# Optimization experiments

Hardware: AMD Instinct MI355X
Metric: run time of the kernel (lower is better)

Reference implementation:

```python
import jax, jax.numpy as jnp
import numpy as np

N, E, M = 100000, 3200000, 1000000  # nodes, message edges, scored move edges
DIN, H = 128, 64


def setup_inputs() -> dict:
    key = jax.random.key(0)
    ks = jax.random.split(key, 20)
    rn = lambda k, shape, s=0.05: (jax.random.normal(k, shape, jnp.float32) * s)
    return {
        "x": jax.random.normal(ks[0], (N, DIN), jnp.float32),
        "edge_index": jax.random.randint(ks[1], (2, E), 0, N, jnp.int64),
        "move_edge_index": jax.random.randint(ks[2], (2, M), 0, N, jnp.int64),
        "lin1_w": rn(ks[3], (DIN, H)), "lin1_b": jnp.zeros((H,), jnp.float32),
        "lin2_w": rn(ks[4], (H, H)), "lin2_b": jnp.zeros((H,), jnp.float32),
        "conv1_wl": rn(ks[5], (H, H)), "conv1_bl": jnp.zeros((H,), jnp.float32),
        "conv1_wr": rn(ks[6], (H, H)),
        "conv2_wl": rn(ks[7], (H, H)), "conv2_bl": jnp.zeros((H,), jnp.float32),
        "conv2_wr": rn(ks[8], (H, H)),
        "mlp_w1": rn(ks[9], (2 * H, H)), "mlp_b1": jnp.zeros((H,), jnp.float32),
        "mlp_w2": rn(ks[10], (H, 1)), "mlp_b2": jnp.zeros((1,), jnp.float32),
    }


def reference(x, edge_index, move_edge_index,
              lin1_w, lin1_b, lin2_w, lin2_b,
              conv1_wl, conv1_bl, conv1_wr,
              conv2_wl, conv2_bl, conv2_wr,
              mlp_w1, mlp_b1, mlp_w2, mlp_b2):
    n = x.shape[0]
    src, dst = edge_index[0], edge_index[1]
    # mean-aggregation degrees (PyG SAGEConv default aggr='mean'; isolated nodes -> 0)
    deg = jax.ops.segment_sum(jnp.ones(src.shape, x.dtype), dst, num_segments=n)
    inv_deg = (jnp.where(deg > 0, 1.0 / jnp.maximum(deg, 1.0), 0.0))[:, None]

    def sage(h, wl, bl, wr):
        # out = W_l @ mean_j h_j + b_l + W_r @ h_i
        agg = jax.ops.segment_sum(h[src], dst, num_segments=n) * inv_deg
        return agg @ wl + bl + h @ wr

    h = jax.nn.relu(x @ lin1_w + lin1_b)
    h = jax.nn.relu(sage(h, conv1_wl, conv1_bl, conv1_wr))
    h = jax.nn.relu(h @ lin2_w + lin2_b)
    h = jax.nn.relu(sage(h, conv2_wl, conv2_bl, conv2_wr))

    # edge scoring: gather src/dst embeddings, concat, 2-layer MLP, tanh
    cat = jnp.concatenate([h[move_edge_index[0]], h[move_edge_index[1]]], axis=1)  # [M, 2H]
    logits = (jax.nn.relu(cat @ mlp_w1 + mlp_b1) @ mlp_w2 + mlp_b2).reshape(-1)
    return jnp.tanh(logits)
```

## Files before the change

kernel.cpp:

```cpp
#include <hip/hip_runtime.h>
#include <math.h>

#define MAXB 512
#define PART_BS 1024
#define NBLK_MAX 248
#define CAPB 96

typedef _Float16 f16;
typedef __attribute__((ext_vector_type(2))) _Float16 f16x2;
typedef __attribute__((ext_vector_type(4))) _Float16 f16x4;
typedef __attribute__((ext_vector_type(8))) _Float16 f16x8;
typedef __attribute__((ext_vector_type(4))) float f32x4;

static __device__ __forceinline__ unsigned short f2h(float f) {
    f16 h = (f16)f; return *(unsigned short*)&h;
}

__global__ __launch_bounds__(PART_BS) void k_part(
    const int* __restrict__ src, const int* __restrict__ dst,
    unsigned* __restrict__ bb, int* __restrict__ cnt,
    const float* __restrict__ lin1_w, const float* __restrict__ c1_wl,
    const float* __restrict__ c1_wr, const float* __restrict__ lin2_w,
    const float* __restrict__ c2_wl, const float* __restrict__ c2_wr,
    const float* __restrict__ mlp_w1, const float* __restrict__ mlp_w2,
    unsigned short* __restrict__ Wt,
    int E, int shift, int pcap, int nblk, int nb) {
    __shared__ int h[MAXB];
    const int blk = blockIdx.x;
    for (int i = blk * PART_BS + (int)threadIdx.x; i < 36928; i += gridDim.x * PART_BS) {
        float v;
        if (i < 8192)       { int j = i;         int n = j >> 7, k = j & 127; v = lin1_w[k * 64 + n]; }
        else if (i < 16384) { int j = i - 8192;  int n = j >> 7, k = j & 127;
                              v = (k < 64) ? c1_wl[k * 64 + n] : c1_wr[(k - 64) * 64 + n]; }
        else if (i < 20480) { int j = i - 16384; int n = j >> 6, k = j & 63;  v = lin2_w[k * 64 + n]; }
        else if (i < 28672) { int j = i - 20480; int n = j >> 7, k = j & 127;
                              v = (k < 64) ? c2_wl[k * 64 + n] : c2_wr[(k - 64) * 64 + n]; }
        else if (i < 32768) { int j = i - 28672; int n = j >> 6, k = j & 63;  v = mlp_w1[k * 64 + n]; }
        else if (i < 36864) { int j = i - 32768; int n = j >> 6, k = j & 63;  v = mlp_w1[(k + 64) * 64 + n]; }
        else                { v = mlp_w2[i - 36864]; }
        Wt[i] = f2h(v);
    }
    const int b0 = blk * pcap;
    const int e1 = min(b0 + pcap, E);
    for (int i = threadIdx.x; i < MAXB; i += PART_BS) h[i] = 0;
    __syncthreads();
    const unsigned mask = (1u << shift) - 1u;
    for (int pos = b0 + (int)threadIdx.x * 8; pos < e1; pos += PART_BS * 8) {
        if (pos + 8 <= e1) {
            int4 d0 = *(const int4*)(dst + pos), d1 = *(const int4*)(dst + pos + 4);
            int4 s0 = *(const int4*)(src + pos), s1 = *(const int4*)(src + pos + 4);
            int dd[8] = {d0.x, d0.y, d0.z, d0.w, d1.x, d1.y, d1.z, d1.w};
            int ss[8] = {s0.x, s0.y, s0.z, s0.w, s1.x, s1.y, s1.z, s1.w};
#pragma unroll
            for (int k = 0; k < 8; ++k) {
                int b = dd[k] >> shift;
                int r = atomicAdd(&h[b], 1);
                if (r < CAPB)
                    bb[((size_t)b * nblk + blk) * CAPB + r] =
                        ((unsigned)ss[k] << shift) | ((unsigned)dd[k] & mask);
            }
        } else {
            for (int k = 0; pos + k < e1; ++k) {
                int d = dst[pos + k];
                int b = d >> shift;
                int r = atomicAdd(&h[b], 1);
                if (r < CAPB)
                    bb[((size_t)b * nblk + blk) * CAPB + r] =
                        ((unsigned)src[pos + k] << shift) | ((unsigned)d & mask);
            }
        }
    }
    __syncthreads();
    for (int i = threadIdx.x; i < nb; i += PART_BS)
        cnt[(size_t)i * nblk + blk] = min(h[i], CAPB);
}

__global__ __launch_bounds__(512) void k_bfmm(
    const unsigned* __restrict__ bb, const int* __restrict__ cnt,
    int* __restrict__ row_st, int* __restrict__ row_en,
    float* __restrict__ inv_deg, int* __restrict__ csr,
    int N, int shift, int CAP, int nblk, int nbB,
    const float* __restrict__ x, const unsigned short* __restrict__ Wtg,
    const float* __restrict__ bias, unsigned short* __restrict__ outh) {
    __shared__ alignas(16) unsigned char smem[64 * 136 * 2];
    const int t = threadIdx.x;

    if (blockIdx.x < (unsigned)nbB) {
        int* deg  = (int*)smem;
        int* cur  = deg + 512;
        int* s    = cur + 512;
        int* scnt = s + 512;
        int b = blockIdx.x;
        int lo = b << shift;
        int hi = min(N, (b + 1) << shift);
        int nn = hi - lo;
        unsigned off = (unsigned)b * CAP;
        unsigned mask = (1u << shift) - 1u;
        const unsigned* seg = bb + (size_t)b * nblk * CAPB;

        for (int i = t; i < nblk; i += 512) scnt[i] = cnt[(size_t)b * nblk + i];
        deg[t] = 0;
        __syncthreads();
        const int tot8 = (nblk * CAPB) >> 3;
        for (int q8 = t; q8 < tot8; q8 += 512) {
            int i = q8 << 3;
            int si = i / CAPB;
            int r = i - si * CAPB;
            int sc = scnt[si];
            if (r < sc) {
                uint4 wA = *(const uint4*)&seg[i];
                uint4 wB = *(const uint4*)&seg[i + 4];
                int nv = min(sc - r, 8);
                unsigned ww[8] = {wA.x, wA.y, wA.z, wA.w, wB.x, wB.y, wB.z, wB.w};
#pragma unroll
                for (int k = 0; k < 8; ++k)
                    if (k < nv) atomicAdd(&deg[ww[k] & mask], 1);
            }
        }
        __syncthreads();
        int d = deg[t];
        int pd = (d + 31) & ~31;
        s[t] = pd;
        __syncthreads();
        for (int o = 1; o < 512; o <<= 1) {
            int u = (t >= o) ? s[t - o] : 0;
            __syncthreads();
            s[t] += u;
            __syncthreads();
        }
        int excl = min(s[t] - pd, CAP);
        int pe = min(excl + pd, CAP);
        cur[t] = excl;
        if (t < nn) {
            row_st[lo + t] = (int)off + excl;
            row_en[lo + t] = (int)off + pe;
            inv_deg[lo + t] = d > 0 ? 1.0f / (float)d : 0.0f;
            for (int j = excl + d; j < pe; ++j) csr[off + j] = N;
        }
        __syncthreads();
        for (int q8 = t; q8 < tot8; q8 += 512) {
            int i = q8 << 3;
            int si = i / CAPB;
            int r = i - si * CAPB;
            int sc = scnt[si];
            if (r < sc) {
                uint4 wA = *(const uint4*)&seg[i];
                uint4 wB = *(const uint4*)&seg[i + 4];
                int nv = min(sc - r, 8);
                unsigned ww[8] = {wA.x, wA.y, wA.z, wA.w, wB.x, wB.y, wB.z, wB.w};
#pragma unroll
                for (int k = 0; k < 8; ++k)
                    if (k < nv) {
                        int dl = (int)(ww[k] & mask);
                        int pos = atomicAdd(&cur[dl], 1);
                        if (pos < CAP) csr[off + pos] = (int)(ww[k] >> shift);
                    }
            }
        }
    } else {
        unsigned short* sW = (unsigned short*)smem;
        const int mb = blockIdx.x - nbB;
        const int row0 = mb * 128;
        const int n = N;
        if (mb == 0 && t < 8)
            ((uint4*)(outh + (size_t)n * 64))[t] = (uint4){0, 0, 0, 0};
        for (int i = t; i < 64 * 16; i += 512) {
            int nn = i >> 4, c = i & 15;
            *(uint4*)&sW[(nn * 17 + c) * 8] = *(const uint4*)&Wtg[i * 8];
        }
        __syncthreads();
        const int lane = t & 63, w = t >> 6;
        const int m = lane & 15, q = lane >> 4;
        const int gr = min(row0 + 16 * w + m, n - 1);
        const float* ar = x + (size_t)gr * 128;
        f32x4 acc[4];
#pragma unroll
        for (int c = 0; c < 4; ++c) acc[c] = (f32x4){0.f, 0.f, 0.f, 0.f};
#pragma unroll
        for (int kk = 0; kk < 4; ++kk) {
            float4 a0 = *(const float4*)(ar + kk * 32 + q * 8);
            float4 a1 = *(const float4*)(ar + kk * 32 + q * 8 + 4);
            f16x8 af;
            af[0] = (f16)a0.x; af[1] = (f16)a0.y; af[2] = (f16)a0.z; af[3] = (f16)a0.w;
            af[4] = (f16)a1.x; af[5] = (f16)a1.y; af[6] = (f16)a1.z; af[7] = (f16)a1.w;
#pragma unroll
            for (int c = 0; c < 4; ++c) {
                f16x8 bf = *(const f16x8*)&sW[((16 * c + m) * 17 + (kk * 4 + q)) * 8];
                acc[c] = __builtin_amdgcn_mfma_f32_16x16x32_f16(af, bf, acc[c], 0, 0, 0);
            }
        }
#pragma unroll
        for (int c = 0; c < 4; ++c) {
            int col = 16 * c + m;
            float bv = bias[col];
#pragma unroll
            for (int i = 0; i < 4; ++i) {
                int r = row0 + 16 * w + q * 4 + i;
                if (r < n) outh[(size_t)r * 64 + col] = f2h(fmaxf(acc[c][i] + bv, 0.f));
            }
        }
    }
}

__global__ __launch_bounds__(256) void k_gather_h(
    const _Float16* __restrict__ hh, const int* __restrict__ csr,
    const int* __restrict__ row_st, const int* __restrict__ row_en,
    const float* __restrict__ inv_deg, _Float16* __restrict__ out, int n) {
    int node = (blockIdx.x * 256 + (int)threadIdx.x) >> 6;
    if (node >= n) return;
    int lane = threadIdx.x & 63;
    int g = lane >> 3, sub = lane & 7;
    int base = row_st[node], end = row_en[node];
    float a[8] = {0.f, 0.f, 0.f, 0.f, 0.f, 0.f, 0.f, 0.f};
#if __has_builtin(__builtin_amdgcn_fdot2)
    const f16x2 one2 = {(f16)1.f, (f16)1.f};
#endif
    for (; base + 64 <= end; base += 64) {
        int4 sA = *(const int4*)&csr[base + 4 * g];
        int4 sB = *(const int4*)&csr[base + 32 + 4 * g];
        int sidx[8] = {sA.x, sA.y, sA.z, sA.w, sB.x, sB.y, sB.z, sB.w};
        f16x8 u[8];
#pragma unroll
        for (int t = 0; t < 8; ++t)
            u[t] = *(const f16x8*)(hh + (((unsigned)sidx[t] << 6) + ((unsigned)sub << 3)));
#if __has_builtin(__builtin_amdgcn_fdot2)
#pragma unroll
        for (int t = 0; t < 8; t += 2)
#pragma unroll
            for (int j = 0; j < 8; ++j) {
                f16x2 v = {u[t][j], u[t + 1][j]};
                a[j] = __builtin_amdgcn_fdot2(v, one2, a[j], false);
            }
#else
#pragma unroll
        for (int t = 0; t < 8; ++t)
#pragma unroll
            for (int j = 0; j < 8; ++j) a[j] += (float)u[t][j];
#endif
    }
    if (base < end) {
        int4 sA = *(const int4*)&csr[base + 4 * g];
        int sidx[4] = {sA.x, sA.y, sA.z, sA.w};
        f16x8 u[4];
#pragma unroll
        for (int t = 0; t < 4; ++t)
            u[t] = *(const f16x8*)(hh + (((unsigned)sidx[t] << 6) + ((unsigned)sub << 3)));
#if __has_builtin(__builtin_amdgcn_fdot2)
#pragma unroll
        for (int t = 0; t < 4; t += 2)
#pragma unroll
            for (int j = 0; j < 8; ++j) {
                f16x2 v = {u[t][j], u[t + 1][j]};
                a[j] = __builtin_amdgcn_fdot2(v, one2, a[j], false);
            }
#else
#pragma unroll
        for (int t = 0; t < 4; ++t)
#pragma unroll
            for (int j = 0; j < 8; ++j) a[j] += (float)u[t][j];
#endif
    }
#pragma unroll
    for (int j = 0; j < 8; ++j) {
        a[j] += __shfl_xor(a[j], 8, 64);
        a[j] += __shfl_xor(a[j], 16, 64);
        a[j] += __shfl_xor(a[j], 32, 64);
    }
    if (g == 0) {
        float idv = inv_deg[node];
        f16x8 o;
#pragma unroll
        for (int j = 0; j < 8; ++j) o[j] = (f16)(a[j] * idv);
        *(f16x8*)(out + (((unsigned)node << 6) + ((unsigned)sub << 3))) = o;
    }
}

__global__ __launch_bounds__(256) void k_mm23(
    const unsigned short* __restrict__ aggH, const unsigned short* __restrict__ h1,
    const unsigned short* __restrict__ Wcg, const float* __restrict__ bl,
    const unsigned short* __restrict__ Wl2g, const float* __restrict__ b2,
    unsigned short* __restrict__ outh, int n) {
    __shared__ alignas(16) unsigned short sm[64 * 72 + 64 * 136];
    unsigned short* hA = sm;
    unsigned short* sW = sm + 64 * 72;
    const int tid = threadIdx.x;
    const int row0 = blockIdx.x * 64;
    for (int i = tid; i < 64 * 16; i += 256) {
        int nn = i >> 4, c = i & 15;
        *(uint4*)&sW[(nn * 17 + c) * 8] = *(const uint4*)&Wcg[i * 8];
    }
    __syncthreads();
    const int lane = tid & 63, w = tid >> 6;
    const int m = lane & 15, q = lane >> 4;
    const int gr = min(row0 + 16 * w + m, n - 1);
    f32x4 acc[4];
#pragma unroll
    for (int c = 0; c < 4; ++c) acc[c] = (f32x4){0.f, 0.f, 0.f, 0.f};
#pragma unroll
    for (int kk = 0; kk < 4; ++kk) {
        const unsigned short* ap = (kk < 2)
            ? (aggH + (size_t)gr * 64 + kk * 32 + q * 8)
            : (h1 + (size_t)gr * 64 + (kk - 2) * 32 + q * 8);
        f16x8 af = *(const f16x8*)ap;
#pragma unroll
        for (int c = 0; c < 4; ++c) {
            f16x8 bf = *(const f16x8*)&sW[((16 * c + m) * 17 + (kk * 4 + q)) * 8];
            acc[c] = __builtin_amdgcn_mfma_f32_16x16x32_f16(af, bf, acc[c], 0, 0, 0);
        }
    }
#pragma unroll
    for (int c = 0; c < 4; ++c) {
        int col = 16 * c + m;
        float bv = bl[col];
#pragma unroll
        for (int i = 0; i < 4; ++i)
            hA[(16 * w + q * 4 + i) * 72 + col] = f2h(fmaxf(acc[c][i] + bv, 0.f));
    }
    __syncthreads();
    for (int i = tid; i < 64 * 8; i += 256) {
        int nn = i >> 3, c = i & 7;
        *(uint4*)&sW[(nn * 9 + c) * 8] = *(const uint4*)&Wl2g[i * 8];
    }
    __syncthreads();
    f32x4 acc2[4];
#pragma unroll
    for (int c = 0; c < 4; ++c) acc2[c] = (f32x4){0.f, 0.f, 0.f, 0.f};
#pragma unroll
    for (int kk = 0; kk < 2; ++kk) {
        f16x8 af = *(const f16x8*)&hA[(16 * w + m) * 72 + kk * 32 + q * 8];
#pragma unroll
        for (int c = 0; c < 4; ++c) {
            f16x8 bf = *(const f16x8*)&sW[((16 * c + m) * 9 + (kk * 4 + q)) * 8];
            acc2[c] = __builtin_amdgcn_mfma_f32_16x16x32_f16(af, bf, acc2[c], 0, 0, 0);
        }
    }
#pragma unroll
    for (int c = 0; c < 4; ++c) {
        int col = 16 * c + m;
        float bv = b2[col];
#pragma unroll
        for (int i = 0; i < 4; ++i) {
            int r = row0 + 16 * w + q * 4 + i;
            if (r < n) outh[(size_t)r * 64 + col] = f2h(fmaxf(acc2[c][i] + bv, 0.f));
        }
    }
}

__global__ __launch_bounds__(256) void k_mm456(
    const unsigned short* __restrict__ aggH, const unsigned short* __restrict__ h3,
    const unsigned short* __restrict__ Wcg, const float* __restrict__ bl,
    const unsigned short* __restrict__ Wpg, const unsigned short* __restrict__ Wqg,
    const float* __restrict__ b1, unsigned short* __restrict__ Ph,
    unsigned short* __restrict__ Qh, int n) {
    __shared__ alignas(16) unsigned short sm[64 * 72 + 2 * 64 * 72];
    unsigned short* hA = sm;
    unsigned short* sW = sm + 64 * 72;
    const int tid = threadIdx.x;
    const int row0 = blockIdx.x * 64;
    for (int i = tid; i < 64 * 16; i += 256) {
        int nn = i >> 4, c = i & 15;
        *(uint4*)&sW[(nn * 17 + c) * 8] = *(const uint4*)&Wcg[i * 8];
    }
    __syncthreads();
    const int lane = tid & 63, w = tid >> 6;
    const int m = lane & 15, q = lane >> 4;
    const int gr = min(row0 + 16 * w + m, n - 1);
    f32x4 acc[4];
#pragma unroll
    for (int c = 0; c < 4; ++c) acc[c] = (f32x4){0.f, 0.f, 0.f, 0.f};
#pragma unroll
    for (int kk = 0; kk < 4; ++kk) {
        const unsigned short* ap = (kk < 2)
            ? (aggH + (size_t)gr * 64 + kk * 32 + q * 8)
            : (h3 + (size_t)gr * 64 + (kk - 2) * 32 + q * 8);
        f16x8 af = *(const f16x8*)ap;
#pragma unroll
        for (int c = 0; c < 4; ++c) {
            f16x8 bf = *(const f16x8*)&sW[((16 * c + m) * 17 + (kk * 4 + q)) * 8];
            acc[c] = __builtin_amdgcn_mfma_f32_16x16x32_f16(af, bf, acc[c], 0, 0, 0);
        }
    }
#pragma unroll
    for (int c = 0; c < 4; ++c) {
        int col = 16 * c + m;
        float bv = bl[col];
#pragma unroll
        for (int i = 0; i < 4; ++i)
            hA[(16 * w + q * 4 + i) * 72 + col] = f2h(fmaxf(acc[c][i] + bv, 0.f));
    }
    __syncthreads();
    for (int i = tid; i < 64 * 8; i += 256) {
        int nn = i >> 3, c = i & 7;
        *(uint4*)&sW[(nn * 9 + c) * 8] = *(const uint4*)&Wpg[i * 8];
        *(uint4*)&sW[4608 + (nn * 9 + c) * 8] = *(const uint4*)&Wqg[i * 8];
    }
    __syncthreads();
    f32x4 accP[4], accQ[4];
#pragma unroll
    for (int c = 0; c < 4; ++c) {
        accP[c] = (f32x4){0.f, 0.f, 0.f, 0.f};
        accQ[c] = (f32x4){0.f, 0.f, 0.f, 0.f};
    }
#pragma unroll
    for (int kk = 0; kk < 2; ++kk) {
        f16x8 af = *(const f16x8*)&hA[(16 * w + m) * 72 + kk * 32 + q * 8];
#pragma unroll
        for (int c = 0; c < 4; ++c) {
            f16x8 bp = *(const f16x8*)&sW[((16 * c + m) * 9 + (kk * 4 + q)) * 8];
            f16x8 bq = *(const f16x8*)&sW[4608 + ((16 * c + m) * 9 + (kk * 4 + q)) * 8];
            accP[c] = __builtin_amdgcn_mfma_f32_16x16x32_f16(af, bp, accP[c], 0, 0, 0);
            accQ[c] = __builtin_amdgcn_mfma_f32_16x16x32_f16(af, bq, accQ[c], 0, 0, 0);
        }
    }
#pragma unroll
    for (int c = 0; c < 4; ++c) {
        int col = 16 * c + m;
        float bv = b1[col];
#pragma unroll
        for (int i = 0; i < 4; ++i) {
            int r = row0 + 16 * w + q * 4 + i;
            if (r < n) {
                Ph[(size_t)r * 64 + col] = f2h(accP[c][i] + bv);
                Qh[(size_t)r * 64 + col] = f2h(accQ[c][i]);
            }
        }
    }
}

__global__ __launch_bounds__(256) void k_score_h(
    const _Float16* __restrict__ P, const _Float16* __restrict__ Q,
    const int* __restrict__ msrc, const int* __restrict__ mdst,
    const _Float16* __restrict__ w2h, const float* __restrict__ b2,
    float* __restrict__ out, int M) {
    int gid = blockIdx.x * 256 + threadIdx.x;
    int e = gid >> 3;
    if (e >= M) return;
    int l = gid & 7;
    int s = msrc[e], d = mdst[e];
    f16x8 p = *(const f16x8*)(P + (((unsigned)s << 6) + ((unsigned)l << 3)));
    f16x8 q = *(const f16x8*)(Q + (((unsigned)d << 6) + ((unsigned)l << 3)));
    f16x8 w = *(const f16x8*)(w2h + ((unsigned)l << 3));
    f16x8 u = p + q;
    f16x8 z = {(f16)0, (f16)0, (f16)0, (f16)0, (f16)0, (f16)0, (f16)0, (f16)0};
    u = __builtin_elementwise_max(u, z);
    float partial;
#if __has_builtin(__builtin_amdgcn_fdot2)
    f16x2 u01 = {u[0], u[1]}, u23 = {u[2], u[3]}, u45 = {u[4], u[5]}, u67 = {u[6], u[7]};
    f16x2 w01 = {w[0], w[1]}, w23 = {w[2], w[3]}, w45 = {w[4], w[5]}, w67 = {w[6], w[7]};
    partial = __builtin_amdgcn_fdot2(u01, w01,
              __builtin_amdgcn_fdot2(u23, w23,
              __builtin_amdgcn_fdot2(u45, w45,
              __builtin_amdgcn_fdot2(u67, w67, 0.f, false), false), false), false);
#else
    partial = 0.f;
#pragma unroll
    for (int i = 0; i < 8; ++i) partial += (float)u[i] * (float)w[i];
#endif
    partial += __shfl_xor(partial, 1, 8);
    partial += __shfl_xor(partial, 2, 8);
    partial += __shfl_xor(partial, 4, 8);
    if (l == 0) {
        float xx = partial + b2[0];
        float t = __expf(2.f * xx);
        out[e] = (t - 1.f) / (t + 1.f);
    }
}

extern "C" void kernel_launch(void* const* d_in, const int* in_sizes, int n_in,
                              void* d_out, int out_size, void* d_ws, size_t ws_size,
                              hipStream_t stream) {
    const float* x      = (const float*)d_in[0];
    const int*   ei     = (const int*)d_in[1];
    const int*   mei    = (const int*)d_in[2];
    const float* lin1_w = (const float*)d_in[3];
    const float* lin1_b = (const float*)d_in[4];
    const float* lin2_w = (const float*)d_in[5];
    const float* lin2_b = (const float*)d_in[6];
    const float* c1_wl  = (const float*)d_in[7];
    const float* c1_bl  = (const float*)d_in[8];
    const float* c1_wr  = (const float*)d_in[9];
    const float* c2_wl  = (const float*)d_in[10];
    const float* c2_bl  = (const float*)d_in[11];
    const float* c2_wr  = (const float*)d_in[12];
    const float* mlp_w1 = (const float*)d_in[13];
    const float* mlp_b1 = (const float*)d_in[14];
    const float* mlp_w2 = (const float*)d_in[15];
    const float* mlp_b2 = (const float*)d_in[16];

    const int N = in_sizes[0] / 128;
    const int E = in_sizes[1] / 2;
    const int M = in_sizes[2] / 2;
    const int* src  = ei;
    const int* dstE = ei + E;
    const int* msrc = mei;
    const int* mdst = mei + M;

    int shift = 8;
    while ((((N - 1) >> shift) + 1) > MAXB) ++shift;
    const int nbuckets = ((N - 1) >> shift) + 1;
    long long avg = (((long long)E << shift) / N) + 1;
    int CAP = (int)((2 * avg + 2047) & ~1023LL);

    const size_t N64 = (size_t)N * 64;
    unsigned short* Hh   = (unsigned short*)d_ws;
    unsigned short* aggH = Hh + N64 + 64;
    unsigned short* Qh   = aggH + N64;
    float* inv_deg = (float*)(Qh + N64);
    int*   row_st  = (int*)(inv_deg + N);
    int*   row_en  = row_st + N;
    int*   cnt     = row_en + N;
    unsigned short* Wt = (unsigned short*)(cnt + (size_t)nbuckets * NBLK_MAX);
    int*   csr     = (int*)(Wt + 36928 + 32);
    float* outf = (float*)d_out;

    unsigned* bb_fresh = (unsigned*)(csr + (size_t)nbuckets * CAP);
    size_t used = (size_t)((char*)bb_fresh - (char*)d_ws);
    size_t need = (size_t)NBLK_MAX * nbuckets * CAPB * 4;
    unsigned* bb;
    int nblk;
    if (ws_size >= used + need) {
        bb = bb_fresh;
        nblk = NBLK_MAX;
    } else {
        bb = (unsigned*)aggH;
        const size_t aliasBytes = (size_t)4 * N64;
        nblk = NBLK_MAX;
        while (nblk > 1 && (size_t)nblk * nbuckets * CAPB * 4 > aliasBytes) --nblk;
    }
    int pcap = (((E + nblk - 1) / nblk) + 7) & ~7;
    nblk = (E + pcap - 1) / pcap;

    const int nbN = (N + 63) / 64;
    const int nbM1 = (N + 127) / 128;
    const int nbM = (int)(((long long)M * 8 + 255) / 256);
    const int nbG = (int)(((long long)N * 64 + 255) / 256);

    k_part<<<nblk, PART_BS, 0, stream>>>(src, dstE, bb, cnt,
                                         lin1_w, c1_wl, c1_wr, lin2_w,
                                         c2_wl, c2_wr, mlp_w1, mlp_w2, Wt,
                                         E, shift, pcap, nblk, nbuckets);

    k_bfmm<<<nbuckets + nbM1, 512, 0, stream>>>(bb, cnt, row_st, row_en,
                                                inv_deg, csr, N, shift, CAP,
                                                nblk, nbuckets,
                                                x, Wt + 0, lin1_b, Hh);

    k_gather_h<<<nbG, 256, 0, stream>>>((const _Float16*)Hh, csr, row_st, row_en,
                                        inv_deg, (_Float16*)aggH, N);
    k_mm23<<<nbN, 256, 0, stream>>>(aggH, Hh, Wt + 8192, c1_bl,
                                    Wt + 16384, lin2_b, Hh, N);

    k_gather_h<<<nbG, 256, 0, stream>>>((const _Float16*)Hh, csr, row_st, row_en,
                                        inv_deg, (_Float16*)aggH, N);
    k_mm456<<<nbN, 256, 0, stream>>>(aggH, Hh, Wt + 20480, c2_bl,
                                     Wt + 28672, Wt + 32768, mlp_b1,
                                     Hh, Qh, N);

    k_score_h<<<nbM, 256, 0, stream>>>((const _Float16*)Hh, (const _Float16*)Qh,
                                       msrc, mdst, (const _Float16*)(Wt + 36864),
                                       mlp_b2, outf, M);
}
```

Before: 364.7 us.

## Fuse neighbor gather-mean into following SAGE matmul kernels via shared-memory tile

Merges the CSR gather/mean-aggregation kernel with the subsequent dense MFMA matmul kernel, so each block aggregates its 64 nodes into shared memory and immediately uses them as the A operand. This drops the aggH round trip through global memory and two kernel launches. Buffers ping-pong between Hh and aggH, with a zeroed sentinel row added for padding. The cost is that each block now serializes 16 nodes per wave during the gather, which changes latency hiding and occupancy, since the larger LDS footprint may reduce resident blocks.

```diff
diff --git a/kernel.cpp b/kernel.cpp
--- a/kernel.cpp
+++ b/kernel.cpp
@@ -202,95 +202,103 @@
     }
 }
 
-__global__ __launch_bounds__(256) void k_gather_h(
+__global__ __launch_bounds__(256) void k_gmm(
     const _Float16* __restrict__ hh, const int* __restrict__ csr,
     const int* __restrict__ row_st, const int* __restrict__ row_en,
-    const float* __restrict__ inv_deg, _Float16* __restrict__ out, int n) {
-    int node = (blockIdx.x * 256 + (int)threadIdx.x) >> 6;
-    if (node >= n) return;
-    int lane = threadIdx.x & 63;
-    int g = lane >> 3, sub = lane & 7;
-    int base = row_st[node], end = row_en[node];
-    float a[8] = {0.f, 0.f, 0.f, 0.f, 0.f, 0.f, 0.f, 0.f};
+    const float* __restrict__ inv_deg,
+    const unsigned short* __restrict__ Wcg, const float* __restrict__ bl,
+    const unsigned short* __restrict__ Wag, const unsigned short* __restrict__ Wbg,
+    const float* __restrict__ b2,
+    unsigned short* __restrict__ outA, unsigned short* __restrict__ outB,
+    int n, int zeroSent) {
+    __shared__ alignas(16) unsigned short hAgg[64 * 72];
+    __shared__ alignas(16) unsigned short hA[64 * 72];
+    __shared__ alignas(16) unsigned short sW[9216];
+    const int t = threadIdx.x;
+    const int row0 = blockIdx.x * 64;
+    const int w = t >> 6, lane = t & 63;
+
+    if (zeroSent && blockIdx.x == 0 && t < 8)
+        ((uint4*)(outA + (size_t)n * 64))[t] = (uint4){0, 0, 0, 0};
+
+    for (int i = t; i < 64 * 16; i += 256) {
+        int nn_ = i >> 4, c = i & 15;
+        *(uint4*)&sW[(nn_ * 17 + c) * 8] = *(const uint4*)&Wcg[i * 8];
+    }
+
+    {
+        int g = lane >> 3, sub = lane & 7;
 #if __has_builtin(__builtin_amdgcn_fdot2)
-    const f16x2 one2 = {(f16)1.f, (f16)1.f};
+        const f16x2 one2 = {(f16)1.f, (f16)1.f};
 #endif
-    for (; base + 64 <= end; base += 64) {
-        int4 sA = *(const int4*)&csr[base + 4 * g];
-        int4 sB = *(const int4*)&csr[base + 32 + 4 * g];
-        int sidx[8] = {sA.x, sA.y, sA.z, sA.w, sB.x, sB.y, sB.z, sB.w};
-        f16x8 u[8];
-#pragma unroll
-        for (int t = 0; t < 8; ++t)
-            u[t] = *(const f16x8*)(hh + (((unsigned)sidx[t] << 6) + ((unsigned)sub << 3)));
+        for (int it = 0; it < 16; ++it) {
+            int node = row0 + it * 4 + w;
+            float a[8] = {0.f, 0.f, 0.f, 0.f, 0.f, 0.f, 0.f, 0.f};
+            if (node < n) {
+                int base = row_st[node], end = row_en[node];
+                for (; base + 64 <= end; base += 64) {
+                    int4 sA = *(const int4*)&csr[base + 4 * g];
+                    int4 sB = *(const int4*)&csr[base + 32 + 4 * g];
+                    int sidx[8] = {sA.x, sA.y, sA.z, sA.w, sB.x, sB.y, sB.z, sB.w};
+                    f16x8 u[8];
+#pragma unroll
+                    for (int tt = 0; tt < 8; ++tt)
+                        u[tt] = *(const f16x8*)(hh + (((unsigned)sidx[tt] << 6) + ((unsigned)sub << 3)));
 #if __has_builtin(__builtin_amdgcn_fdot2)
 #pragma unroll
-        for (int t = 0; t < 8; t += 2)
+                    for (int tt = 0; tt < 8; tt += 2)
+#pragma unroll
+                        for (int j = 0; j < 8; ++j) {
+                            f16x2 v = {u[tt][j], u[tt + 1][j]};
+                            a[j] = __builtin_amdgcn_fdot2(v, one2, a[j], false);
+                        }
+#else
+#pragma unroll
+                    for (int tt = 0; tt < 8; ++tt)
+#pragma unroll
+                        for (int j = 0; j < 8; ++j) a[j] += (float)u[tt][j];
+#endif
+                }
+                if (base < end) {
+                    int4 sA = *(const int4*)&csr[base + 4 * g];
+                    int sidx[4] = {sA.x, sA.y, sA.z, sA.w};
+                    f16x8 u[4];
+#pragma unroll
+                    for (int tt = 0; tt < 4; ++tt)
+                        u[tt] = *(const f16x8*)(hh + (((unsigned)sidx[tt] << 6) + ((unsigned)sub << 3)));
+#if __has_builtin(__builtin_amdgcn_fdot2)
+#pragma unroll
+                    for (int tt = 0; tt < 4; tt += 2)
+#pragma unroll
+                        for (int j = 0; j < 8; ++j) {
+                            f16x2 v = {u[tt][j], u[tt + 1][j]};
+                            a[j] = __builtin_amdgcn_fdot2(v, one2, a[j], false);
+                        }
+#else
+#pragma unroll
+                    for (int tt = 0; tt < 4; ++tt)
+#pragma unroll
+                        for (int j = 0; j < 8; ++j) a[j] += (float)u[tt][j];
+#endif
+                }
+            }
 #pragma unroll
             for (int j = 0; j < 8; ++j) {
-                f16x2 v = {u[t][j], u[t + 1][j]};
-                a[j] = __builtin_amdgcn_fdot2(v, one2, a[j], false);
-            }
-#else
-#pragma unroll
-        for (int t = 0; t < 8; ++t)
-#pragma unroll
-            for (int j = 0; j < 8; ++j) a[j] += (float)u[t][j];
-#endif
-    }
-    if (base < end) {
-        int4 sA = *(const int4*)&csr[base + 4 * g];
-        int sidx[4] = {sA.x, sA.y, sA.z, sA.w};
-        f16x8 u[4];
-#pragma unroll
-        for (int t = 0; t < 4; ++t)
-            u[t] = *(const f16x8*)(hh + (((unsigned)sidx[t] << 6) + ((unsigned)sub << 3)));
-#if __has_builtin(__builtin_amdgcn_fdot2)
-#pragma unroll
-        for (int t = 0; t < 4; t += 2)
-#pragma unroll
-            for (int j = 0; j < 8; ++j) {
-                f16x2 v = {u[t][j], u[t + 1][j]};
-                a[j] = __builtin_amdgcn_fdot2(v, one2, a[j], false);
-            }
-#else
-#pragma unroll
-        for (int t = 0; t < 4; ++t)
-#pragma unroll
-            for (int j = 0; j < 8; ++j) a[j] += (float)u[t][j];
-#endif
-    }
-#pragma unroll
-    for (int j = 0; j < 8; ++j) {
-        a[j] += __shfl_xor(a[j], 8, 64);
-        a[j] += __shfl_xor(a[j], 16, 64);
-        a[j] += __shfl_xor(a[j], 32, 64);
-    }
-    if (g == 0) {
-        float idv = inv_deg[node];
-        f16x8 o;
-#pragma unroll
-        for (int j = 0; j < 8; ++j) o[j] = (f16)(a[j] * idv);
-        *(f16x8*)(out + (((unsigned)node << 6) + ((unsigned)sub << 3))) = o;
-    }
-}
-
-__global__ __launch_bounds__(256) void k_mm23(
-    const unsigned short* __restrict__ aggH, const unsigned short* __restrict__ h1,
-    const unsigned short* __restrict__ Wcg, const float* __restrict__ bl,
-    const unsigned short* __restrict__ Wl2g, const float* __restrict__ b2,
-    unsigned short* __restrict__ outh, int n) {
-    __shared__ alignas(16) unsigned short sm[64 * 72 + 64 * 136];
-    unsigned short* hA = sm;
-    unsigned short* sW = sm + 64 * 72;
-    const int tid = threadIdx.x;
-    const int row0 = blockIdx.x * 64;
-    for (int i = tid; i < 64 * 16; i += 256) {
-        int nn = i >> 4, c = i & 15;
-        *(uint4*)&sW[(nn * 17 + c) * 8] = *(const uint4*)&Wcg[i * 8];
+                a[j] += __shfl_xor(a[j], 8, 64);
+                a[j] += __shfl_xor(a[j], 16, 64);
+                a[j] += __shfl_xor(a[j], 32, 64);
+            }
+            if (g == 0) {
+                float idv = (node < n) ? inv_deg[node] : 0.f;
+                f16x8 o;
+#pragma unroll
+                for (int j = 0; j < 8; ++j) o[j] = (f16)(a[j] * idv);
+                *(f16x8*)&hAgg[(it * 4 + w) * 72 + sub * 8] = o;
+            }
+        }
     }
     __syncthreads();
-    const int lane = tid & 63, w = tid >> 6;
+
     const int m = lane & 15, q = lane >> 4;
     const int gr = min(row0 + 16 * w + m, n - 1);
     f32x4 acc[4];
@@ -298,10 +306,9 @@
     for (int c = 0; c < 4; ++c) acc[c] = (f32x4){0.f, 0.f, 0.f, 0.f};
 #pragma unroll
     for (int kk = 0; kk < 4; ++kk) {
-        const unsigned short* ap = (kk < 2)
-            ? (aggH + (size_t)gr * 64 + kk * 32 + q * 8)
-            : (h1 + (size_t)gr * 64 + (kk - 2) * 32 + q * 8);
-        f16x8 af = *(const f16x8*)ap;
+        f16x8 af = (kk < 2)
+            ? *(const f16x8*)&hAgg[(16 * w + m) * 72 + kk * 32 + q * 8]
+            : *(const f16x8*)(hh + (size_t)gr * 64 + (kk - 2) * 32 + q * 8);
 #pragma unroll
         for (int c = 0; c < 4; ++c) {
             f16x8 bf = *(const f16x8*)&sW[((16 * c + m) * 17 + (kk * 4 + q)) * 8];
@@ -317,111 +324,73 @@
             hA[(16 * w + q * 4 + i) * 72 + col] = f2h(fmaxf(acc[c][i] + bv, 0.f));
     }
     __syncthreads();
-    for (int i = tid; i < 64 * 8; i += 256) {
-        int nn = i >> 3, c = i & 7;
-        *(uint4*)&sW[(nn * 9 + c) * 8] = *(const uint4*)&Wl2g[i * 8];
+
+    if (outB) {
+        for (int i = t; i < 64 * 8; i += 256) {
+            int nn_ = i >> 3, c = i & 7;
+            *(uint4*)&sW[(nn_ * 9 + c) * 8] = *(const uint4*)&Wag[i * 8];
+            *(uint4*)&sW[4608 + (nn_ * 9 + c) * 8] = *(const uint4*)&Wbg[i * 8];
+        }
+    } else {
+        for (int i = t; i < 64 * 8; i += 256) {
+            int nn_ = i >> 3, c = i & 7;
+            *(uint4*)&sW[(nn_ * 9 + c) * 8] = *(const uint4*)&Wag[i * 8];
+        }
     }
     __syncthreads();
-    f32x4 acc2[4];
-#pragma unroll
-    for (int c = 0; c < 4; ++c) acc2[c] = (f32x4){0.f, 0.f, 0.f, 0.f};
-#pragma unroll
-    for (int kk = 0; kk < 2; ++kk) {
-        f16x8 af = *(const f16x8*)&hA[(16 * w + m) * 72 + kk * 32 + q * 8];
+
+    if (outB) {
+        f32x4 accP[4], accQ[4];
 #pragma unroll
         for (int c = 0; c < 4; ++c) {
-            f16x8 bf = *(const f16x8*)&sW[((16 * c + m) * 9 + (kk * 4 + q)) * 8];
-            acc2[c] = __builtin_amdgcn_mfma_f32_16x16x32_f16(af, bf, acc2[c], 0, 0, 0);
-        }
-    }
-#pragma unroll
-    for (int c = 0; c < 4; ++c) {
-        int col = 16 * c + m;
-        float bv = b2[col];
-#pragma unroll
-        for (int i = 0; i < 4; ++i) {
-            int r = row0 + 16 * w + q * 4 + i;
-            if (r < n) outh[(size_t)r * 64 + col] = f2h(fmaxf(acc2[c][i] + bv, 0.f));
-        }
-    }
-}
-
-__global__ __launch_bounds__(256) void k_mm456(
-    const unsigned short* __restrict__ aggH, const unsigned short* __restrict__ h3,
-    const unsigned short* __restrict__ Wcg, const float* __restrict__ bl,
-    const unsigned short* __restrict__ Wpg, const unsigned short* __restrict__ Wqg,
-    const float* __restrict__ b1, unsigned short* __restrict__ Ph,
-    unsigned short* __restrict__ Qh, int n) {
-    __shared__ alignas(16) unsigned short sm[64 * 72 + 2 * 64 * 72];
-    unsigned short* hA = sm;
-    unsigned short* sW = sm + 64 * 72;
-    const int tid = threadIdx.x;
-    const int row0 = blockIdx.x * 64;
-    for (int i = tid; i < 64 * 16; i += 256) {
-        int nn = i >> 4, c = i & 15;
-        *(uint4*)&sW[(nn * 17 + c) * 8] = *(const uint4*)&Wcg[i * 8];
-    }
-    __syncthreads();
-    const int lane = tid & 63, w = tid >> 6;
-    const int m = lane & 15, q = lane >> 4;
-    const int gr = min(row0 + 16 * w + m, n - 1);
-    f32x4 acc[4];
-#pragma unroll
-    for (int c = 0; c < 4; ++c) acc[c] = (f32x4){0.f, 0.f, 0.f, 0.f};
-#pragma unroll
-    for (int kk = 0; kk < 4; ++kk) {
-        const unsigned short* ap = (kk < 2)
-            ? (aggH + (size_t)gr * 64 + kk * 32 + q * 8)
-            : (h3 + (size_t)gr * 64 + (kk - 2) * 32 + q * 8);
-        f16x8 af = *(const f16x8*)ap;
+            accP[c] = (f32x4){0.f, 0.f, 0.f, 0.f};
+            accQ[c] = (f32x4){0.f, 0.f, 0.f, 0.f};
+        }
+#pragma unroll
+        for (int kk = 0; kk < 2; ++kk) {
+            f16x8 af = *(const f16x8*)&hA[(16 * w + m) * 72 + kk * 32 + q * 8];
+#pragma unroll
+            for (int c = 0; c < 4; ++c) {
+                f16x8 bp = *(const f16x8*)&sW[((16 * c + m) * 9 + (kk * 4 + q)) * 8];
+                f16x8 bq = *(const f16x8*)&sW[4608 + ((16 * c + m) * 9 + (kk * 4 + q)) * 8];
+                accP[c] = __builtin_amdgcn_mfma_f32_16x16x32_f16(af, bp, accP[c], 0, 0, 0);
+                accQ[c] = __builtin_amdgcn_mfma_f32_16x16x32_f16(af, bq, accQ[c], 0, 0, 0);
+            }
+        }
 #pragma unroll
         for (int c = 0; c < 4; ++c) {
-            f16x8 bf = *(const f16x8*)&sW[((16 * c + m) * 17 + (kk * 4 + q)) * 8];
-            acc[c] = __builtin_amdgcn_mfma_f32_16x16x32_f16(af, bf, acc[c], 0, 0, 0);
-        }
-    }
-#pragma unroll
-    for (int c = 0; c < 4; ++c) {
-        int col = 16 * c + m;
-        float bv = bl[col];
-#pragma unroll
-        for (int i = 0; i < 4; ++i)
-            hA[(16 * w + q * 4 + i) * 72 + col] = f2h(fmaxf(acc[c][i] + bv, 0.f));
-    }
-    __syncthreads();
-    for (int i = tid; i < 64 * 8; i += 256) {
-        int nn = i >> 3, c = i & 7;
-        *(uint4*)&sW[(nn * 9 + c) * 8] = *(const uint4*)&Wpg[i * 8];
-        *(uint4*)&sW[4608 + (nn * 9 + c) * 8] = *(const uint4*)&Wqg[i * 8];
-    }
-    __syncthreads();
-    f32x4 accP[4], accQ[4];
-#pragma unroll
-    for (int c = 0; c < 4; ++c) {
-        accP[c] = (f32x4){0.f, 0.f, 0.f, 0.f};
-        accQ[c] = (f32x4){0.f, 0.f, 0.f, 0.f};
-    }
-#pragma unroll
-    for (int kk = 0; kk < 2; ++kk) {
-        f16x8 af = *(const f16x8*)&hA[(16 * w + m) * 72 + kk * 32 + q * 8];
+            int col = 16 * c + m;
+            float bv = b2[col];
+#pragma unroll
+            for (int i = 0; i < 4; ++i) {
+                int r = row0 + 16 * w + q * 4 + i;
+                if (r < n) {
+                    outA[(size_t)r * 64 + col] = f2h(accP[c][i] + bv);
+                    outB[(size_t)r * 64 + col] = f2h(accQ[c][i]);
+                }
+            }
+        }
+    } else {
+        f32x4 acc2[4];
+#pragma unroll
+        for (int c = 0; c < 4; ++c) acc2[c] = (f32x4){0.f, 0.f, 0.f, 0.f};
+#pragma unroll
+        for (int kk = 0; kk < 2; ++kk) {
+            f16x8 af = *(const f16x8*)&hA[(16 * w + m) * 72 + kk * 32 + q * 8];
+#pragma unroll
+            for (int c = 0; c < 4; ++c) {
+                f16x8 bf = *(const f16x8*)&sW[((16 * c + m) * 9 + (kk * 4 + q)) * 8];
+                acc2[c] = __builtin_amdgcn_mfma_f32_16x16x32_f16(af, bf, acc2[c], 0, 0, 0);
+            }
+        }
 #pragma unroll
         for (int c = 0; c < 4; ++c) {
-            f16x8 bp = *(const f16x8*)&sW[((16 * c + m) * 9 + (kk * 4 + q)) * 8];
-            f16x8 bq = *(const f16x8*)&sW[4608 + ((16 * c + m) * 9 + (kk * 4 + q)) * 8];
-            accP[c] = __builtin_amdgcn_mfma_f32_16x16x32_f16(af, bp, accP[c], 0, 0, 0);
-            accQ[c] = __builtin_amdgcn_mfma_f32_16x16x32_f16(af, bq, accQ[c], 0, 0, 0);
-        }
-    }
-#pragma unroll
-    for (int c = 0; c < 4; ++c) {
-        int col = 16 * c + m;
-        float bv = b1[col];
-#pragma unroll
-        for (int i = 0; i < 4; ++i) {
-            int r = row0 + 16 * w + q * 4 + i;
-            if (r < n) {
-                Ph[(size_t)r * 64 + col] = f2h(accP[c][i] + bv);
-                Qh[(size_t)r * 64 + col] = f2h(accQ[c][i]);
+            int col = 16 * c + m;
+            float bv = b2[col];
+#pragma unroll
+            for (int i = 0; i < 4; ++i) {
+                int r = row0 + 16 * w + q * 4 + i;
+                if (r < n) outA[(size_t)r * 64 + col] = f2h(fmaxf(acc2[c][i] + bv, 0.f));
             }
         }
     }
@@ -504,7 +473,7 @@
     const size_t N64 = (size_t)N * 64;
     unsigned short* Hh   = (unsigned short*)d_ws;
     unsigned short* aggH = Hh + N64 + 64;
-    unsigned short* Qh   = aggH + N64;
+    unsigned short* Qh   = aggH + N64 + 64;
     float* inv_deg = (float*)(Qh + N64);
     int*   row_st  = (int*)(inv_deg + N);
     int*   row_en  = row_st + N;
@@ -533,7 +502,6 @@
     const int nbN = (N + 63) / 64;
     const int nbM1 = (N + 127) / 128;
     const int nbM = (int)(((long long)M * 8 + 255) / 256);
-    const int nbG = (int)(((long long)N * 64 + 255) / 256);
 
     k_part<<<nblk, PART_BS, 0, stream>>>(src, dstE, bb, cnt,
                                          lin1_w, c1_wl, c1_wr, lin2_w,
@@ -545,16 +513,15 @@
                                                 nblk, nbuckets,
                                                 x, Wt + 0, lin1_b, Hh);
 
-    k_gather_h<<<nbG, 256, 0, stream>>>((const _Float16*)Hh, csr, row_st, row_en,
-                                        inv_deg, (_Float16*)aggH, N);
-    k_mm23<<<nbN, 256, 0, stream>>>(aggH, Hh, Wt + 8192, c1_bl,
-                                    Wt + 16384, lin2_b, Hh, N);
-
-    k_gather_h<<<nbG, 256, 0, stream>>>((const _Float16*)Hh, csr, row_st, row_en,
-                                        inv_deg, (_Float16*)aggH, N);
-    k_mm456<<<nbN, 256, 0, stream>>>(aggH, Hh, Wt + 20480, c2_bl,
-                                     Wt + 28672, Wt + 32768, mlp_b1,
-                                     Hh, Qh, N);
+    k_gmm<<<nbN, 256, 0, stream>>>((const _Float16*)Hh, csr, row_st, row_en,
+                                   inv_deg, Wt + 8192, c1_bl,
+                                   Wt + 16384, nullptr, lin2_b,
+                                   aggH, nullptr, N, 1);
+
+    k_gmm<<<nbN, 256, 0, stream>>>((const _Float16*)aggH, csr, row_st, row_en,
+                                   inv_deg, Wt + 20480, c2_bl,
+                                   Wt + 28672, Wt + 32768, mlp_b1,
+                                   Hh, Qh, N, 0);
 
     k_score_h<<<nbM, 256, 0, stream>>>((const _Float16*)Hh, (const _Float16*)Qh,
                                        msrc, mdst, (const _Float16*)(Wt + 36864),
```

Measured after the change: 381.6 us. 1.05x slower.
